# Kernel optimization log

Hardware: AMD Instinct MI355X
Metric: run time of the kernel (lower is better)

The kernel has to match this reference:

```python
import jax, jax.numpy as jnp
import numpy as np

N_NODES = 50000
N_EDGES = 1600000
F_IN = 128
HID = 32
HEADS = 4
N_CLS = 2
NEG_SLOPE = 0.2


def gat_conv(x, src, dst, W, a_src, a_dst, b, heads, ch, n):
    # x: [N, F_in]; W: [F_in, heads*ch]; a_src/a_dst: [heads, ch]; b: [heads*ch]
    h = (x @ W).reshape(n, heads, ch)                      # [N, H, C]
    alpha_s = jnp.einsum('nhc,hc->nh', h, a_src)           # [N, H]
    alpha_d = jnp.einsum('nhc,hc->nh', h, a_dst)           # [N, H]
    e = jax.nn.leaky_relu(alpha_s[src] + alpha_d[dst], NEG_SLOPE)  # [E, H]
    m = jax.ops.segment_max(e, dst, num_segments=n)        # [N, H]
    ex = jnp.exp(e - m[dst])                               # [E, H]
    denom = jax.ops.segment_sum(ex, dst, num_segments=n)   # [N, H]
    alpha = ex / denom[dst]                                # [E, H]
    msg = h[src] * alpha[:, :, None]                       # [E, H, C]
    out = jax.ops.segment_sum(msg, dst, num_segments=n)    # [N, H, C]
    return out.reshape(n, heads * ch) + b


def setup_inputs() -> dict:
    key = jax.random.key(0)
    ks = jax.random.split(key, 16)
    g = lambda k, shp, fan: jax.random.normal(k, shp, jnp.float32) * (1.0 / np.sqrt(fan))
    x = jax.random.normal(ks[0], (N_NODES, F_IN), jnp.float32)
    edge_index = jax.random.randint(ks[1], (2, N_EDGES), 0, N_NODES, jnp.int32)
    return {
        'x': x,
        'edge_index': edge_index,
        'W1': g(ks[2], (F_IN, HEADS * HID), F_IN),
        'a1s': g(ks[3], (HEADS, HID), HID),
        'a1d': g(ks[4], (HEADS, HID), HID),
        'b1': jnp.zeros((HEADS * HID,), jnp.float32),
        'W2': g(ks[5], (HEADS * HID, HEADS * HID), HEADS * HID),
        'a2s': g(ks[6], (HEADS, HID), HID),
        'a2d': g(ks[7], (HEADS, HID), HID),
        'b2': jnp.zeros((HEADS * HID,), jnp.float32),
        'W3': g(ks[8], (HEADS * HID, HID), HEADS * HID),
        'a3s': g(ks[9], (1, HID), HID),
        'a3d': g(ks[10], (1, HID), HID),
        'b3': jnp.zeros((HID,), jnp.float32),
        'Wlin': g(ks[11], (HID, N_CLS), HID),
        'blin': jnp.zeros((N_CLS,), jnp.float32),
    }


def reference(x, edge_index, W1, a1s, a1d, b1, W2, a2s, a2d, b2, W3, a3s, a3d, b3, Wlin, blin):
    n = x.shape[0]
    # PyG GATConv default: add self-loops
    loop = jnp.arange(n, dtype=edge_index.dtype)
    src = jnp.concatenate([edge_index[0], loop])
    dst = jnp.concatenate([edge_index[1], loop])
    h = gat_conv(x, src, dst, W1, a1s, a1d, b1, HEADS, HID, n)
    h = jax.nn.relu(h)
    h = gat_conv(h, src, dst, W2, a2s, a2d, b2, HEADS, HID, n)
    h = jax.nn.relu(h)
    h = gat_conv(h, src, dst, W3, a3s, a3d, b3, 1, HID, n)
    h = jax.nn.relu(h)
    return h @ Wlin + blin
```

## Files before the change

### kernel.cpp

```cpp
#include <hip/hip_runtime.h>

#define NEG 0.2f
#define BSH 8
#define CHB 8192
__device__ __forceinline__ float lrelu(float x){ return fmaxf(x, NEG*x); }

__device__ __forceinline__ float bf2f(unsigned short u){
  union{unsigned int i; float f;} v; v.i = ((unsigned int)u)<<16; return v.f;
}
__device__ __forceinline__ unsigned short f2bf(float f){
  union{float f; unsigned int i;} v; v.f = f;
  unsigned int b = v.i;
  b += 0x7FFFu + ((b>>16)&1u);
  return (unsigned short)(b>>16);
}

__global__ __launch_bounds__(256) void zero_kernel(int* __restrict__ p, int n){
  int i = blockIdx.x*256 + threadIdx.x;
  if (i < n) p[i] = 0;
}

__global__ __launch_bounds__(256) void bin_count(const int* __restrict__ dstv, int* __restrict__ bcnt,
                                                 int E, int NB){
  __shared__ int lh[256];
  int tid = threadIdx.x;
  lh[tid] = 0;
  __syncthreads();
  int e0 = blockIdx.x * CHB;
  int e1 = min(e0 + CHB, E);
  for (int i = e0 + tid; i < e1; i += 256)
    atomicAdd(&lh[dstv[i] >> BSH], 1);
  __syncthreads();
  if (tid < NB && lh[tid] > 0) atomicAdd(&bcnt[tid], lh[tid]);
}

__global__ __launch_bounds__(256) void scan_kernel(const int* __restrict__ counts, int* __restrict__ offs,
                                                   int* __restrict__ cursor, int n){
  __shared__ int wsum[4];
  __shared__ int carry_s;
  int tid = threadIdx.x, lane = tid & 63, wv = tid >> 6;
  if (tid == 0) carry_s = 0;
  __syncthreads();
  const int CH = 2048;
  int nch = (n + CH - 1)/CH;
  for (int ch=0; ch<nch; ++ch){
    int base_i = ch*CH + tid*8;
    int v[8], pre[8];
    #pragma unroll
    for (int j=0;j<8;++j){ int i=base_i+j; v[j]=(i<n)?counts[i]:0; }
    int t=0;
    #pragma unroll
    for (int j=0;j<8;++j){ pre[j]=t; t+=v[j]; }
    int incl=t;
    #pragma unroll
    for (int m=1;m<64;m<<=1){ int u=__shfl_up(incl,m); if(lane>=m) incl+=u; }
    int wexcl = incl - t;
    if (lane==63) wsum[wv]=incl;
    __syncthreads();
    int wbase=0;
    for (int w2=0;w2<wv;++w2) wbase+=wsum[w2];
    int total = wsum[0]+wsum[1]+wsum[2]+wsum[3];
    int base = carry_s + wbase + wexcl;
    #pragma unroll
    for (int j=0;j<8;++j){ int i=base_i+j; if(i<n){ int val=base+pre[j]; offs[i]=val; cursor[i]=val; } }
    __syncthreads();
    if (tid==0) carry_s += total;
    __syncthreads();
  }
  if (tid==0) offs[n]=carry_s;
}

__global__ __launch_bounds__(256) void bin_scatter(const int* __restrict__ srcv, const int* __restrict__ dstv,
                                                   int* __restrict__ bcur, int2* __restrict__ pairs,
                                                   int E, int NB){
  __shared__ int lh[256];
  __shared__ int lcur[256];
  int tid = threadIdx.x;
  lh[tid] = 0;
  __syncthreads();
  int e0 = blockIdx.x * CHB;
  int e1 = min(e0 + CHB, E);
  for (int i = e0 + tid; i < e1; i += 256)
    atomicAdd(&lh[dstv[i] >> BSH], 1);
  __syncthreads();
  if (tid < NB){
    int c = lh[tid];
    lcur[tid] = (c > 0) ? atomicAdd(&bcur[tid], c) : 0;
  }
  __syncthreads();
  for (int i = e0 + tid; i < e1; i += 256){
    int s = srcv[i], d = dstv[i];
    int p = atomicAdd(&lcur[d >> BSH], 1);
    pairs[p] = make_int2(s, d);
  }
}

__global__ __launch_bounds__(256) void bucket_finalize(const int2* __restrict__ pairs,
                                                       const int* __restrict__ bbase,
                                                       int* __restrict__ offs, int* __restrict__ csr,
                                                       int N, int E){
  __shared__ int lh[256];
  __shared__ int lcur[256];
  __shared__ int wsum[4];
  int b = blockIdx.x;
  int base = bbase[b], end = bbase[b+1];
  int node0 = b << BSH;
  int tid = threadIdx.x, lane = tid & 63, wv = tid >> 6;
  lh[tid] = 0;
  if (b == 0 && tid == 0) offs[N] = E;
  __syncthreads();
  for (int i = base + tid; i < end; i += 256)
    atomicAdd(&lh[pairs[i].y - node0], 1);
  __syncthreads();
  {
    int v = lh[tid];
    int incl = v;
    #pragma unroll
    for (int m=1;m<64;m<<=1){ int u=__shfl_up(incl,m); if(lane>=m) incl+=u; }
    if (lane==63) wsum[wv]=incl;
    __syncthreads();
    int wbase=0;
    for (int w2=0;w2<wv;++w2) wbase+=wsum[w2];
    int excl = wbase + incl - v;
    lcur[tid] = base + excl;
    int node = node0 + tid;
    if (node < N) offs[node] = base + excl;
  }
  __syncthreads();
  for (int i = base + tid; i < end; i += 256){
    int2 pr = pairs[i];
    int p = atomicAdd(&lcur[pr.y - node0], 1);
    csr[p] = pr.x;
  }
}

template<int NOUT, int TR, int HEADS>
__global__ __launch_bounds__(256) void gemm_fused(const float* __restrict__ X, const float* __restrict__ W,
    const float* __restrict__ a_s, const float* __restrict__ a_d,
    unsigned short* __restrict__ hb, float* __restrict__ as_, float* __restrict__ ad_, int n){
  constexpr int NC = NOUT / 8;
  constexpr int RG = 256 / NC;
  constexpr int BM = RG * TR;
  constexpr int CHK = (NOUT > 64) ? 64 : 128;
  constexpr int NCH = 128 / CHK;
  __shared__ float Wl[CHK * NOUT];
  int tid = threadIdx.x;
  int cg = tid % NC;
  int rg = tid / NC;
  int lane = tid & 63;
  int row0 = blockIdx.x * BM + rg * TR;
  const float4* Wv = (const float4*)W;
  const float4* Xv = (const float4*)X;
  float acc[TR][8];
  #pragma unroll
  for (int r=0;r<TR;++r)
    #pragma unroll
    for (int c=0;c<8;++c) acc[r][c]=0.f;
  for (int ch = 0; ch < NCH; ++ch){
    if (ch) __syncthreads();
    for (int i = tid; i < CHK*NOUT/4; i += 256)
      ((float4*)Wl)[i] = Wv[ch*(CHK*NOUT/4) + i];
    __syncthreads();
    for (int k4i = 0; k4i < CHK/4; ++k4i){
      int k4 = ch*(CHK/4) + k4i;
      float4 xv[TR];
      #pragma unroll
      for (int r = 0; r < TR; ++r){
        int row = row0 + r;
        xv[r] = (row < n) ? Xv[(size_t)row*32 + k4] : make_float4(0.f,0.f,0.f,0.f);
      }
      #pragma unroll
      for (int kk = 0; kk < 4; ++kk){
        float wv[8];
        #pragma unroll
        for (int c = 0; c < 8; ++c) wv[c] = Wl[(k4i*4+kk)*NOUT + cg*8 + c];
        #pragma unroll
        for (int r = 0; r < TR; ++r){
          float xr = (kk==0)?xv[r].x:(kk==1)?xv[r].y:(kk==2)?xv[r].z:xv[r].w;
          #pragma unroll
          for (int c = 0; c < 8; ++c) acc[r][c] = fmaf(xr, wv[c], acc[r][c]);
        }
      }
    }
  }
  float asl[8], adl[8];
  #pragma unroll
  for (int c=0;c<8;++c){ asl[c]=a_s[cg*8+c]; adl[c]=a_d[cg*8+c]; }
  #pragma unroll
  for (int r = 0; r < TR; ++r){
    int row = row0 + r;
    float s=0.f, dd=0.f;
    #pragma unroll
    for (int c=0;c<8;++c){ s = fmaf(acc[r][c], asl[c], s); dd = fmaf(acc[r][c], adl[c], dd); }
    s  += __shfl_xor(s,1);  s  += __shfl_xor(s,2);
    dd += __shfl_xor(dd,1); dd += __shfl_xor(dd,2);
    if (HEADS == 4){
      int base = lane & ~15;
      float s0=__shfl(s,base),  s1=__shfl(s,base+4),  s2=__shfl(s,base+8),  s3=__shfl(s,base+12);
      float d0=__shfl(dd,base), d1=__shfl(dd,base+4), d2=__shfl(dd,base+8), d3=__shfl(dd,base+12);
      if (row < n && cg == 0){
        ((float4*)as_)[row] = make_float4(s0,s1,s2,s3);
        ((float4*)ad_)[row] = make_float4(d0,d1,d2,d3);
      }
    } else {
      if (row < n && (lane&3) == 0){ as_[row] = s; ad_[row] = dd; }
    }
    if (row < n){
      ushort4 p0, p1;
      p0.x=f2bf(acc[r][0]); p0.y=f2bf(acc[r][1]); p0.z=f2bf(acc[r][2]); p0.w=f2bf(acc[r][3]);
      p1.x=f2bf(acc[r][4]); p1.y=f2bf(acc[r][5]); p1.z=f2bf(acc[r][6]); p1.w=f2bf(acc[r][7]);
      *(ushort4*)&hb[(size_t)row*NOUT + cg*8 + 0] = p0;
      *(ushort4*)&hb[(size_t)row*NOUT + cg*8 + 4] = p1;
    }
  }
}

__device__ __forceinline__ float sel4(int hh, float4 v){
  return (hh&2) ? ((hh&1)?v.w:v.z) : ((hh&1)?v.y:v.x);
}

__global__ __launch_bounds__(256) void agg_h4(const unsigned short* __restrict__ hb,
    const float4* __restrict__ as_, const float4* __restrict__ ad_,
    const int* __restrict__ offs, const int* __restrict__ csr,
    const float* __restrict__ bias, float* __restrict__ hout, int n){
  int wid = (blockIdx.x*256 + threadIdx.x) >> 6;
  int lane = threadIdx.x & 63;
  if (wid >= n) return;
  const int d = wid;
  float4 ad4 = ad_[d];
  float4 asd = as_[d];
  int r0 = offs[d], r1 = offs[d+1];
  int half = lane >> 5;
  int cl = lane & 31;
  int hh = cl >> 3;
  float adh = sel4(hh, ad4);
  float asv = sel4(hh, asd);
  float acc0=0.f, acc1=0.f, acc2=0.f, acc3=0.f, den=0.f;
  if (half == 0){
    float w = __expf(lrelu(asv+adh));
    ushort4 hv = *(const ushort4*)&hb[(size_t)d*128 + 4*cl];
    acc0 = w*bf2f(hv.x); acc1 = w*bf2f(hv.y); acc2 = w*bf2f(hv.z); acc3 = w*bf2f(hv.w); den = w;
  }
  int e = r0 + half;
  for (; e+14 < r1; e += 16){
    int s0=csr[e],   s1=csr[e+2],  s2=csr[e+4],  s3=csr[e+6];
    int s4=csr[e+8], s5=csr[e+10], s6=csr[e+12], s7=csr[e+14];
    float4 a0=as_[s0], a1=as_[s1], a2=as_[s2], a3=as_[s3];
    float4 a4=as_[s4], a5=as_[s5], a6=as_[s6], a7=as_[s7];
    ushort4 h0=*(const ushort4*)&hb[(size_t)s0*128+4*cl];
    ushort4 h1=*(const ushort4*)&hb[(size_t)s1*128+4*cl];
    ushort4 h2=*(const ushort4*)&hb[(size_t)s2*128+4*cl];
    ushort4 h3=*(const ushort4*)&hb[(size_t)s3*128+4*cl];
    ushort4 h4=*(const ushort4*)&hb[(size_t)s4*128+4*cl];
    ushort4 h5=*(const ushort4*)&hb[(size_t)s5*128+4*cl];
    ushort4 h6=*(const ushort4*)&hb[(size_t)s6*128+4*cl];
    ushort4 h7=*(const ushort4*)&hb[(size_t)s7*128+4*cl];
    float w0=__expf(lrelu(sel4(hh,a0)+adh));
    float w1=__expf(lrelu(sel4(hh,a1)+adh));
    float w2=__expf(lrelu(sel4(hh,a2)+adh));
    float w3=__expf(lrelu(sel4(hh,a3)+adh));
    float w4=__expf(lrelu(sel4(hh,a4)+adh));
    float w5=__expf(lrelu(sel4(hh,a5)+adh));
    float w6=__expf(lrelu(sel4(hh,a6)+adh));
    float w7=__expf(lrelu(sel4(hh,a7)+adh));
    acc0=fmaf(w0,bf2f(h0.x),acc0); acc1=fmaf(w0,bf2f(h0.y),acc1); acc2=fmaf(w0,bf2f(h0.z),acc2); acc3=fmaf(w0,bf2f(h0.w),acc3); den+=w0;
    acc0=fmaf(w1,bf2f(h1.x),acc0); acc1=fmaf(w1,bf2f(h1.y),acc1); acc2=fmaf(w1,bf2f(h1.z),acc2); acc3=fmaf(w1,bf2f(h1.w),acc3); den+=w1;
    acc0=fmaf(w2,bf2f(h2.x),acc0); acc1=fmaf(w2,bf2f(h2.y),acc1); acc2=fmaf(w2,bf2f(h2.z),acc2); acc3=fmaf(w2,bf2f(h2.w),acc3); den+=w2;
    acc0=fmaf(w3,bf2f(h3.x),acc0); acc1=fmaf(w3,bf2f(h3.y),acc1); acc2=fmaf(w3,bf2f(h3.z),acc2); acc3=fmaf(w3,bf2f(h3.w),acc3); den+=w3;
    acc0=fmaf(w4,bf2f(h4.x),acc0); acc1=fmaf(w4,bf2f(h4.y),acc1); acc2=fmaf(w4,bf2f(h4.z),acc2); acc3=fmaf(w4,bf2f(h4.w),acc3); den+=w4;
    acc0=fmaf(w5,bf2f(h5.x),acc0); acc1=fmaf(w5,bf2f(h5.y),acc1); acc2=fmaf(w5,bf2f(h5.z),acc2); acc3=fmaf(w5,bf2f(h5.w),acc3); den+=w5;
    acc0=fmaf(w6,bf2f(h6.x),acc0); acc1=fmaf(w6,bf2f(h6.y),acc1); acc2=fmaf(w6,bf2f(h6.z),acc2); acc3=fmaf(w6,bf2f(h6.w),acc3); den+=w6;
    acc0=fmaf(w7,bf2f(h7.x),acc0); acc1=fmaf(w7,bf2f(h7.y),acc1); acc2=fmaf(w7,bf2f(h7.z),acc2); acc3=fmaf(w7,bf2f(h7.w),acc3); den+=w7;
  }
  for (; e < r1; e += 2){
    int s = csr[e];
    float4 a4 = as_[s];
    float w = __expf(lrelu(sel4(hh,a4)+adh));
    ushort4 hv = *(const ushort4*)&hb[(size_t)s*128+4*cl];
    acc0=fmaf(w,bf2f(hv.x),acc0); acc1=fmaf(w,bf2f(hv.y),acc1); acc2=fmaf(w,bf2f(hv.z),acc2); acc3=fmaf(w,bf2f(hv.w),acc3); den+=w;
  }
  acc0 += __shfl_xor(acc0,32); acc1 += __shfl_xor(acc1,32);
  acc2 += __shfl_xor(acc2,32); acc3 += __shfl_xor(acc3,32);
  den  += __shfl_xor(den,32);
  if (half == 0){
    float inv = 1.0f/den;
    float4 bv = *(const float4*)&bias[4*cl];
    float4 o;
    o.x = fmaxf(fmaf(acc0,inv,bv.x), 0.f);
    o.y = fmaxf(fmaf(acc1,inv,bv.y), 0.f);
    o.z = fmaxf(fmaf(acc2,inv,bv.z), 0.f);
    o.w = fmaxf(fmaf(acc3,inv,bv.w), 0.f);
    *(float4*)&hout[(size_t)d*128 + 4*cl] = o;
  }
}

__global__ __launch_bounds__(256) void agg_h1_lin(const unsigned short* __restrict__ hb,
    const float* __restrict__ as_, const float* __restrict__ ad_,
    const int* __restrict__ offs, const int* __restrict__ csr,
    const float* __restrict__ b3, const float* __restrict__ Wlin, const float* __restrict__ blin,
    float* __restrict__ out, int n){
  int wid = (blockIdx.x*256 + threadIdx.x) >> 6;
  int lane = threadIdx.x & 63;
  if (wid >= n) return;
  const int d = wid;
  float add = ad_[d];
  float asd = as_[d];
  int r0 = offs[d], r1 = offs[d+1];
  int half = lane >> 5;
  int c = lane & 31;
  float acc=0.f, den=0.f;
  if (half == 0){
    float w = __expf(lrelu(asd+add));
    acc = w*bf2f(hb[(size_t)d*32 + c]); den = w;
  }
  int e = r0 + half;
  for (; e+14 < r1; e += 16){
    int s0=csr[e],   s1=csr[e+2],  s2=csr[e+4],  s3=csr[e+6];
    int s4=csr[e+8], s5=csr[e+10], s6=csr[e+12], s7=csr[e+14];
    float a0=as_[s0], a1=as_[s1], a2=as_[s2], a3=as_[s3];
    float a4=as_[s4], a5=as_[s5], a6=as_[s6], a7=as_[s7];
    float v0=bf2f(hb[(size_t)s0*32+c]), v1=bf2f(hb[(size_t)s1*32+c]);
    float v2=bf2f(hb[(size_t)s2*32+c]), v3=bf2f(hb[(size_t)s3*32+c]);
    float v4=bf2f(hb[(size_t)s4*32+c]), v5=bf2f(hb[(size_t)s5*32+c]);
    float v6=bf2f(hb[(size_t)s6*32+c]), v7=bf2f(hb[(size_t)s7*32+c]);
    float w0=__expf(lrelu(a0+add)), w1=__expf(lrelu(a1+add));
    float w2=__expf(lrelu(a2+add)), w3=__expf(lrelu(a3+add));
    float w4=__expf(lrelu(a4+add)), w5=__expf(lrelu(a5+add));
    float w6=__expf(lrelu(a6+add)), w7=__expf(lrelu(a7+add));
    acc=fmaf(w0,v0,acc); den+=w0;
    acc=fmaf(w1,v1,acc); den+=w1;
    acc=fmaf(w2,v2,acc); den+=w2;
    acc=fmaf(w3,v3,acc); den+=w3;
    acc=fmaf(w4,v4,acc); den+=w4;
    acc=fmaf(w5,v5,acc); den+=w5;
    acc=fmaf(w6,v6,acc); den+=w6;
    acc=fmaf(w7,v7,acc); den+=w7;
  }
  for (; e < r1; e += 2){
    int s = csr[e];
    float w=__expf(lrelu(as_[s]+add));
    acc=fmaf(w,bf2f(hb[(size_t)s*32+c]),acc); den+=w;
  }
  acc += __shfl_xor(acc,32);
  den += __shfl_xor(den,32);
  float v = fmaxf(acc/den + b3[c], 0.f);
  float y0 = v*Wlin[c*2+0];
  float y1 = v*Wlin[c*2+1];
  #pragma unroll
  for (int mk=16; mk>=1; mk>>=1){ y0 += __shfl_xor(y0,mk); y1 += __shfl_xor(y1,mk); }
  if (lane==0){ out[(size_t)d*2+0] = y0 + blin[0]; out[(size_t)d*2+1] = y1 + blin[1]; }
}

extern "C" void kernel_launch(void* const* d_in, const int* in_sizes, int n_in,
                              void* d_out, int out_size, void* d_ws, size_t ws_size,
                              hipStream_t stream){
  const int N = in_sizes[0] / 128;
  const int E = in_sizes[1] / 2;
  const float* x    = (const float*)d_in[0];
  const int*   ei   = (const int*)d_in[1];
  const int*   srcv = ei;
  const int*   dstv = ei + E;
  const float* W1 = (const float*)d_in[2];
  const float* a1s= (const float*)d_in[3];
  const float* a1d= (const float*)d_in[4];
  const float* b1 = (const float*)d_in[5];
  const float* W2 = (const float*)d_in[6];
  const float* a2s= (const float*)d_in[7];
  const float* a2d= (const float*)d_in[8];
  const float* b2 = (const float*)d_in[9];
  const float* W3 = (const float*)d_in[10];
  const float* a3s= (const float*)d_in[11];
  const float* a3d= (const float*)d_in[12];
  const float* b3 = (const float*)d_in[13];
  const float* Wlin=(const float*)d_in[14];
  const float* blin=(const float*)d_in[15];
  float* out = (float*)d_out;

  const int NB = (N + 255) >> BSH;

  char* wp = (char*)d_ws;
  auto alloc = [&](size_t bytes)->void*{
    void* p = (void*)wp;
    wp += (bytes + 255) & ~(size_t)255;
    return p;
  };
  float* h     = (float*)alloc((size_t)N*128*4);
  unsigned short* hb = (unsigned short*)alloc((size_t)N*128*2);
  float* as_   = (float*)alloc((size_t)N*4*4);
  float* ad_   = (float*)alloc((size_t)N*4*4);
  int*   offs  = (int*)alloc((size_t)(N+1)*4);
  int*   csr   = (int*)alloc((size_t)E*4);
  int*   bcnt  = (int*)alloc((size_t)NB*4);
  int*   bbase = (int*)alloc((size_t)(NB+1)*4);
  int*   bcur  = (int*)alloc((size_t)NB*4);
  int2*  pairs = (int2*)h;

  const int gridB = (E + CHB - 1)/CHB;
  const int gridW = (N + 3)/4;

  zero_kernel<<<1, 256, 0, stream>>>(bcnt, NB);
  bin_count<<<gridB, 256, 0, stream>>>(dstv, bcnt, E, NB);
  scan_kernel<<<1, 256, 0, stream>>>(bcnt, bbase, bcur, NB);
  bin_scatter<<<gridB, 256, 0, stream>>>(srcv, dstv, bcur, pairs, E, NB);
  bucket_finalize<<<NB, 256, 0, stream>>>(pairs, bbase, offs, csr, N, E);

  gemm_fused<128,4,4><<<(N+63)/64, 256, 0, stream>>>(x, W1, a1s, a1d, hb, as_, ad_, N);
  agg_h4<<<gridW, 256, 0, stream>>>(hb, (const float4*)as_, (const float4*)ad_, offs, csr, b1, h, N);

  gemm_fused<128,4,4><<<(N+63)/64, 256, 0, stream>>>(h, W2, a2s, a2d, hb, as_, ad_, N);
  agg_h4<<<gridW, 256, 0, stream>>>(hb, (const float4*)as_, (const float4*)ad_, offs, csr, b2, h, N);

  gemm_fused<32,4,1><<<(N+255)/256, 256, 0, stream>>>(h, W3, a3s, a3d, hb, as_, ad_, N);
  agg_h1_lin<<<gridW, 256, 0, stream>>>(hb, as_, ad_, offs, csr, b3, Wlin, blin, out, N);
}
```

Before: 430.6 us.

## Split 4-head aggregation into per-head kernels with 4-edge-parallel wavefronts

Replaces the single agg_h4 kernel, where a wavefront processed all four heads for a node, with four launches of a templated per-head kernel. Each wavefront now handles one head's 32 channels, with 16 lanes reading 2 bf16 each, and processes 4 edges in parallel per quarter-wave. It also adds nontemporal loads for CSR indices and nontemporal stores for output. The intent is to shrink each pass's gathered working set (64 bytes per source row per head) so it fits better in cache. The cost is reading the CSR, offsets and attention scalars four times and launching four times as many waves.

```diff
diff --git a/kernel.cpp b/kernel.cpp
--- a/kernel.cpp
+++ b/kernel.cpp
@@ -219,7 +219,8 @@
   return (hh&2) ? ((hh&1)?v.w:v.z) : ((hh&1)?v.y:v.x);
 }
 
-__global__ __launch_bounds__(256) void agg_h4(const unsigned short* __restrict__ hb,
+template<int HEAD>
+__global__ __launch_bounds__(256) void agg_head(const unsigned short* __restrict__ hb,
     const float4* __restrict__ as_, const float4* __restrict__ ad_,
     const int* __restrict__ offs, const int* __restrict__ csr,
     const float* __restrict__ bias, float* __restrict__ hout, int n){
@@ -227,70 +228,47 @@
   int lane = threadIdx.x & 63;
   if (wid >= n) return;
   const int d = wid;
-  float4 ad4 = ad_[d];
-  float4 asd = as_[d];
+  int q = lane >> 4;
+  int cl = lane & 15;
+  float adh = sel4(HEAD, ad_[d]);
+  float ash = sel4(HEAD, as_[d]);
   int r0 = offs[d], r1 = offs[d+1];
-  int half = lane >> 5;
-  int cl = lane & 31;
-  int hh = cl >> 3;
-  float adh = sel4(hh, ad4);
-  float asv = sel4(hh, asd);
-  float acc0=0.f, acc1=0.f, acc2=0.f, acc3=0.f, den=0.f;
-  if (half == 0){
-    float w = __expf(lrelu(asv+adh));
-    ushort4 hv = *(const ushort4*)&hb[(size_t)d*128 + 4*cl];
-    acc0 = w*bf2f(hv.x); acc1 = w*bf2f(hv.y); acc2 = w*bf2f(hv.z); acc3 = w*bf2f(hv.w); den = w;
-  }
-  int e = r0 + half;
-  for (; e+14 < r1; e += 16){
-    int s0=csr[e],   s1=csr[e+2],  s2=csr[e+4],  s3=csr[e+6];
-    int s4=csr[e+8], s5=csr[e+10], s6=csr[e+12], s7=csr[e+14];
-    float4 a0=as_[s0], a1=as_[s1], a2=as_[s2], a3=as_[s3];
-    float4 a4=as_[s4], a5=as_[s5], a6=as_[s6], a7=as_[s7];
-    ushort4 h0=*(const ushort4*)&hb[(size_t)s0*128+4*cl];
-    ushort4 h1=*(const ushort4*)&hb[(size_t)s1*128+4*cl];
-    ushort4 h2=*(const ushort4*)&hb[(size_t)s2*128+4*cl];
-    ushort4 h3=*(const ushort4*)&hb[(size_t)s3*128+4*cl];
-    ushort4 h4=*(const ushort4*)&hb[(size_t)s4*128+4*cl];
-    ushort4 h5=*(const ushort4*)&hb[(size_t)s5*128+4*cl];
-    ushort4 h6=*(const ushort4*)&hb[(size_t)s6*128+4*cl];
-    ushort4 h7=*(const ushort4*)&hb[(size_t)s7*128+4*cl];
-    float w0=__expf(lrelu(sel4(hh,a0)+adh));
-    float w1=__expf(lrelu(sel4(hh,a1)+adh));
-    float w2=__expf(lrelu(sel4(hh,a2)+adh));
-    float w3=__expf(lrelu(sel4(hh,a3)+adh));
-    float w4=__expf(lrelu(sel4(hh,a4)+adh));
-    float w5=__expf(lrelu(sel4(hh,a5)+adh));
-    float w6=__expf(lrelu(sel4(hh,a6)+adh));
-    float w7=__expf(lrelu(sel4(hh,a7)+adh));
-    acc0=fmaf(w0,bf2f(h0.x),acc0); acc1=fmaf(w0,bf2f(h0.y),acc1); acc2=fmaf(w0,bf2f(h0.z),acc2); acc3=fmaf(w0,bf2f(h0.w),acc3); den+=w0;
-    acc0=fmaf(w1,bf2f(h1.x),acc0); acc1=fmaf(w1,bf2f(h1.y),acc1); acc2=fmaf(w1,bf2f(h1.z),acc2); acc3=fmaf(w1,bf2f(h1.w),acc3); den+=w1;
-    acc0=fmaf(w2,bf2f(h2.x),acc0); acc1=fmaf(w2,bf2f(h2.y),acc1); acc2=fmaf(w2,bf2f(h2.z),acc2); acc3=fmaf(w2,bf2f(h2.w),acc3); den+=w2;
-    acc0=fmaf(w3,bf2f(h3.x),acc0); acc1=fmaf(w3,bf2f(h3.y),acc1); acc2=fmaf(w3,bf2f(h3.z),acc2); acc3=fmaf(w3,bf2f(h3.w),acc3); den+=w3;
-    acc0=fmaf(w4,bf2f(h4.x),acc0); acc1=fmaf(w4,bf2f(h4.y),acc1); acc2=fmaf(w4,bf2f(h4.z),acc2); acc3=fmaf(w4,bf2f(h4.w),acc3); den+=w4;
-    acc0=fmaf(w5,bf2f(h5.x),acc0); acc1=fmaf(w5,bf2f(h5.y),acc1); acc2=fmaf(w5,bf2f(h5.z),acc2); acc3=fmaf(w5,bf2f(h5.w),acc3); den+=w5;
-    acc0=fmaf(w6,bf2f(h6.x),acc0); acc1=fmaf(w6,bf2f(h6.y),acc1); acc2=fmaf(w6,bf2f(h6.z),acc2); acc3=fmaf(w6,bf2f(h6.w),acc3); den+=w6;
-    acc0=fmaf(w7,bf2f(h7.x),acc0); acc1=fmaf(w7,bf2f(h7.y),acc1); acc2=fmaf(w7,bf2f(h7.z),acc2); acc3=fmaf(w7,bf2f(h7.w),acc3); den+=w7;
-  }
-  for (; e < r1; e += 2){
-    int s = csr[e];
-    float4 a4 = as_[s];
-    float w = __expf(lrelu(sel4(hh,a4)+adh));
-    ushort4 hv = *(const ushort4*)&hb[(size_t)s*128+4*cl];
-    acc0=fmaf(w,bf2f(hv.x),acc0); acc1=fmaf(w,bf2f(hv.y),acc1); acc2=fmaf(w,bf2f(hv.z),acc2); acc3=fmaf(w,bf2f(hv.w),acc3); den+=w;
-  }
-  acc0 += __shfl_xor(acc0,32); acc1 += __shfl_xor(acc1,32);
-  acc2 += __shfl_xor(acc2,32); acc3 += __shfl_xor(acc3,32);
-  den  += __shfl_xor(den,32);
-  if (half == 0){
+  const size_t choff = (size_t)HEAD*32 + 2*cl;
+  float acc0=0.f, acc1=0.f, den=0.f;
+  if (q == 0){
+    float w = __expf(lrelu(ash + adh));
+    unsigned int hv = *(const unsigned int*)&hb[(size_t)d*128 + choff];
+    acc0 = w*bf2f((unsigned short)(hv&0xffffu));
+    acc1 = w*bf2f((unsigned short)(hv>>16));
+    den = w;
+  }
+  for (int e = r0; e < r1; e += 8){
+    int e0 = e + q, e1 = e + 4 + q;
+    bool v0 = e0 < r1, v1 = e1 < r1;
+    int s0 = v0 ? __builtin_nontemporal_load(&csr[e0]) : d;
+    int s1 = v1 ? __builtin_nontemporal_load(&csr[e1]) : d;
+    float4 a0 = as_[s0], a1 = as_[s1];
+    unsigned int h0 = *(const unsigned int*)&hb[(size_t)s0*128 + choff];
+    unsigned int h1 = *(const unsigned int*)&hb[(size_t)s1*128 + choff];
+    float w0 = v0 ? __expf(lrelu(sel4(HEAD,a0)+adh)) : 0.f;
+    float w1 = v1 ? __expf(lrelu(sel4(HEAD,a1)+adh)) : 0.f;
+    acc0 = fmaf(w0, bf2f((unsigned short)(h0&0xffffu)), acc0);
+    acc1 = fmaf(w0, bf2f((unsigned short)(h0>>16)),     acc1);
+    den += w0;
+    acc0 = fmaf(w1, bf2f((unsigned short)(h1&0xffffu)), acc0);
+    acc1 = fmaf(w1, bf2f((unsigned short)(h1>>16)),     acc1);
+    den += w1;
+  }
+  acc0 += __shfl_xor(acc0,16); acc0 += __shfl_xor(acc0,32);
+  acc1 += __shfl_xor(acc1,16); acc1 += __shfl_xor(acc1,32);
+  den  += __shfl_xor(den,16);  den  += __shfl_xor(den,32);
+  if (q == 0){
     float inv = 1.0f/den;
-    float4 bv = *(const float4*)&bias[4*cl];
-    float4 o;
-    o.x = fmaxf(fmaf(acc0,inv,bv.x), 0.f);
-    o.y = fmaxf(fmaf(acc1,inv,bv.y), 0.f);
-    o.z = fmaxf(fmaf(acc2,inv,bv.z), 0.f);
-    o.w = fmaxf(fmaf(acc3,inv,bv.w), 0.f);
-    *(float4*)&hout[(size_t)d*128 + 4*cl] = o;
+    float o0 = fmaxf(fmaf(acc0, inv, bias[HEAD*32 + 2*cl    ]), 0.f);
+    float o1 = fmaxf(fmaf(acc1, inv, bias[HEAD*32 + 2*cl + 1]), 0.f);
+    union { float f[2]; unsigned long long u; } pk;
+    pk.f[0] = o0; pk.f[1] = o1;
+    __builtin_nontemporal_store(pk.u, (unsigned long long*)&hout[(size_t)d*128 + choff]);
   }
 }
 
@@ -405,10 +383,16 @@
   bucket_finalize<<<NB, 256, 0, stream>>>(pairs, bbase, offs, csr, N, E);
 
   gemm_fused<128,4,4><<<(N+63)/64, 256, 0, stream>>>(x, W1, a1s, a1d, hb, as_, ad_, N);
-  agg_h4<<<gridW, 256, 0, stream>>>(hb, (const float4*)as_, (const float4*)ad_, offs, csr, b1, h, N);
+  agg_head<0><<<gridW, 256, 0, stream>>>(hb, (const float4*)as_, (const float4*)ad_, offs, csr, b1, h, N);
+  agg_head<1><<<gridW, 256, 0, stream>>>(hb, (const float4*)as_, (const float4*)ad_, offs, csr, b1, h, N);
+  agg_head<2><<<gridW, 256, 0, stream>>>(hb, (const float4*)as_, (const float4*)ad_, offs, csr, b1, h, N);
+  agg_head<3><<<gridW, 256, 0, stream>>>(hb, (const float4*)as_, (const float4*)ad_, offs, csr, b1, h, N);
 
   gemm_fused<128,4,4><<<(N+63)/64, 256, 0, stream>>>(h, W2, a2s, a2d, hb, as_, ad_, N);
-  agg_h4<<<gridW, 256, 0, stream>>>(hb, (const float4*)as_, (const float4*)ad_, offs, csr, b2, h, N);
+  agg_head<0><<<gridW, 256, 0, stream>>>(hb, (const float4*)as_, (const float4*)ad_, offs, csr, b2, h, N);
+  agg_head<1><<<gridW, 256, 0, stream>>>(hb, (const float4*)as_, (const float4*)ad_, offs, csr, b2, h, N);
+  agg_head<2><<<gridW, 256, 0, stream>>>(hb, (const float4*)as_, (const float4*)ad_, offs, csr, b2, h, N);
+  agg_head<3><<<gridW, 256, 0, stream>>>(hb, (const float4*)as_, (const float4*)ad_, offs, csr, b2, h, N);
 
   gemm_fused<32,4,1><<<(N+255)/256, 256, 0, stream>>>(h, W3, a3s, a3d, hb, as_, ad_, N);
   agg_h1_lin<<<gridW, 256, 0, stream>>>(hb, as_, ad_, offs, csr, b3, Wlin, blin, out, N);
```

New measurement: 576.9 us. 34.0% more time.
